# Performance work log

Hardware: AMD Instinct MI355X
Metric: run time of the kernel (lower is better)

The kernel has to match this reference:

```python
import jax, jax.numpy as jnp
from jax import lax
import numpy as np

A = 9            # anchors per location (3 scales x 3 ratios)
STRIDE = 16      # feat_stride
PRE_NMS = 6000   # top-k proposals before NMS (test mode)
POST_NMS = 300   # proposals kept after NMS (test mode)
NMS_T = 0.7      # NMS IoU threshold
MIN_SIZE = 16.0  # min proposal side length


def _anchor_ref(base=16, ratios=(0.5, 1.0, 2.0), scales=(8, 16, 32)):
    """Standard py-faster-rcnn anchor references, shape (9, 4)."""
    ratios = np.array(ratios, np.float64)
    scales = np.array(scales, np.float64)
    ctr = (base - 1) / 2.0
    size = float(base * base)
    ws = np.round(np.sqrt(size / ratios))
    hs = np.round(ws * ratios)
    ra = np.stack([ctr - 0.5 * (ws - 1), ctr - 0.5 * (hs - 1),
                   ctr + 0.5 * (ws - 1), ctr + 0.5 * (hs - 1)], 1)
    out = []
    for a in ra:
        w = a[2] - a[0] + 1.0
        h = a[3] - a[1] + 1.0
        cx = a[0] + 0.5 * (w - 1)
        cy = a[1] + 0.5 * (h - 1)
        ws2 = w * scales
        hs2 = h * scales
        out.append(np.stack([cx - 0.5 * (ws2 - 1), cy - 0.5 * (hs2 - 1),
                             cx + 0.5 * (ws2 - 1), cy + 0.5 * (hs2 - 1)], 1))
    return jnp.asarray(np.concatenate(out, 0), jnp.float32)


def _nms_keep(boxes):
    """Greedy NMS on score-sorted boxes (N,4) -> bool keep mask (N,)."""
    x1, y1, x2, y2 = boxes[:, 0], boxes[:, 1], boxes[:, 2], boxes[:, 3]
    areas = (x2 - x1 + 1.0) * (y2 - y1 + 1.0)
    iw = jnp.clip(jnp.minimum(x2[:, None], x2[None, :]) - jnp.maximum(x1[:, None], x1[None, :]) + 1.0, 0.0)
    ih = jnp.clip(jnp.minimum(y2[:, None], y2[None, :]) - jnp.maximum(y1[:, None], y1[None, :]) + 1.0, 0.0)
    inter = iw * ih
    iou = inter / (areas[:, None] + areas[None, :] - inter)
    n = boxes.shape[0]
    idx = jnp.arange(n)
    def body(i, keep):
        sup = (iou[i] > NMS_T) & (idx > i)
        return jnp.where(keep[i], keep & ~sup, keep)
    return lax.fori_loop(0, n, body, jnp.ones((n,), bool))


def _rpn_forward(feature_map, W_rpn, b_rpn, W_score, b_score, W_bbox, b_bbox, img_size):
    dn = ('NHWC', 'HWIO', 'NHWC')
    rpn = lax.conv_general_dilated(feature_map, W_rpn, (1, 1), 'SAME', dimension_numbers=dn) + b_rpn
    rpn = jax.nn.relu(rpn)
    cls = lax.conv_general_dilated(rpn, W_score, (1, 1), 'SAME', dimension_numbers=dn) + b_score
    bbx = lax.conv_general_dilated(rpn, W_bbox, (1, 1), 'SAME', dimension_numbers=dn) + b_bbox
    n, h, w, _ = feature_map.shape
    cls = cls.reshape(n, h, w, A, 2)
    prob = jax.nn.softmax(cls, axis=-1)
    fg = prob[..., 1].reshape(-1)           # (h*w*A,) foreground prob
    deltas = bbx.reshape(-1, 4)             # (h*w*A, 4)
    # anchors: shifts over (h, w), anchor-ref inner -> matches (h,w,A) flattening
    ref = _anchor_ref()
    sx = jnp.arange(w, dtype=jnp.float32) * STRIDE
    sy = jnp.arange(h, dtype=jnp.float32) * STRIDE
    ys, xs = jnp.meshgrid(sy, sx, indexing='ij')
    shifts = jnp.stack([xs, ys, xs, ys], -1).reshape(-1, 1, 4)
    anchors = (shifts + ref[None]).reshape(-1, 4)
    # decode deltas -> boxes
    aw = anchors[:, 2] - anchors[:, 0] + 1.0
    ah = anchors[:, 3] - anchors[:, 1] + 1.0
    acx = anchors[:, 0] + 0.5 * aw
    acy = anchors[:, 1] + 0.5 * ah
    pcx = deltas[:, 0] * aw + acx
    pcy = deltas[:, 1] * ah + acy
    pw = jnp.exp(deltas[:, 2]) * aw
    ph = jnp.exp(deltas[:, 3]) * ah
    imh = img_size[0].astype(jnp.float32)
    imw = img_size[1].astype(jnp.float32)
    boxes = jnp.stack([
        jnp.clip(pcx - 0.5 * pw, 0.0, imw - 1.0),
        jnp.clip(pcy - 0.5 * ph, 0.0, imh - 1.0),
        jnp.clip(pcx + 0.5 * pw, 0.0, imw - 1.0),
        jnp.clip(pcy + 0.5 * ph, 0.0, imh - 1.0)], -1)
    # min-size filter
    bw = boxes[:, 2] - boxes[:, 0] + 1.0
    bh = boxes[:, 3] - boxes[:, 1] + 1.0
    fg = jnp.where((bw >= MIN_SIZE) & (bh >= MIN_SIZE), fg, -1e9)
    # pre-NMS top-k (sorted descending)
    top_s, top_i = lax.top_k(fg, PRE_NMS)
    top_b = boxes[top_i]
    keep = _nms_keep(lax.stop_gradient(top_b))
    sel_s = jnp.where(keep, top_s, -1e9)
    _, sel_i = lax.top_k(sel_s, POST_NMS)
    rois = top_b[sel_i]
    ok = keep[sel_i] & (sel_s[sel_i] > -1e8)
    return jnp.where(ok[:, None], rois, 0.0)  # (POST_NMS, 4), zero-padded


def setup_inputs() -> dict:
    key = jax.random.key(0)
    ks = jax.random.split(key, 7)
    C_in, C_mid = 1024, 512
    std = 0.01
    return {
        'feature_map': jax.random.normal(ks[0], (1, 100, 150, C_in), jnp.float32),
        'W_rpn': jax.random.normal(ks[1], (3, 3, C_in, C_mid), jnp.float32) * std,
        'b_rpn': jnp.zeros((C_mid,), jnp.float32),
        'W_score': jax.random.normal(ks[2], (1, 1, C_mid, A * 2), jnp.float32) * std,
        'b_score': jnp.zeros((A * 2,), jnp.float32),
        'W_bbox': jax.random.normal(ks[3], (1, 1, C_mid, A * 4), jnp.float32) * std,
        'b_bbox': jnp.zeros((A * 4,), jnp.float32),
        'img_size': jnp.array([1600, 2400], jnp.int32),
    }


def reference(feature_map, W_rpn, b_rpn, W_score, b_score, W_bbox, b_bbox, img_size):
    return _rpn_forward(feature_map, W_rpn, b_rpn, W_score, b_score, W_bbox, b_bbox, img_size)
```

## Files before the change

### kernel.cpp

```cpp
#include <hip/hip_runtime.h>
#include <hip/hip_bf16.h>

typedef unsigned int u32;
typedef unsigned long long u64;

#define H_FM 100
#define W_FM 150
#define CIN 1024
#define CMID 512
#define NPIX 15000
#define NANCH 135000
#define PRE_NMS_N 6000
#define POST_NMS_N 300
#define WPR 94

typedef __attribute__((ext_vector_type(8))) short short8;
typedef __attribute__((ext_vector_type(8))) __bf16 bf16x8;
typedef __attribute__((ext_vector_type(4))) float f32x4;

__device__ __forceinline__ u32 fkey(float f) {
  u32 u = __float_as_uint(f);
  return (u & 0x80000000u) ? ~u : (u | 0x80000000u);
}

__device__ __forceinline__ u64 shfl64(u64 v, int src) {
  u32 lo = (u32)__shfl((int)(u32)v, src, 64);
  u32 hi = (u32)__shfl((int)(u32)(v >> 32), src, 64);
  return ((u64)hi << 32) | (u64)lo;
}

struct FragArg {
  short8 v;
  __device__ operator short8() const { return v; }
  __device__ operator bf16x8() const { return __builtin_bit_cast(bf16x8, v); }
};
__device__ __forceinline__ f32x4 mfma16(short8 a, short8 b, f32x4 c) {
  return __builtin_amdgcn_mfma_f32_16x16x32_bf16(FragArg{a}, FragArg{b}, c, 0, 0, 0);
}

#define GLL(gp, lp) __builtin_amdgcn_global_load_lds(                        \
    (const __attribute__((address_space(1))) unsigned int*)(gp),             \
    (__attribute__((address_space(3))) unsigned int*)(lp), 16, 0, 0)

__device__ __forceinline__ void split3(float f, unsigned short& a,
                                       unsigned short& b, unsigned short& c) {
  __hip_bfloat16 h0 = __float2bfloat16(f);
  float f0 = __bfloat162float(h0);
  float r1 = f - f0;
  __hip_bfloat16 h1 = __float2bfloat16(r1);
  float r2 = r1 - __bfloat162float(h1);
  __hip_bfloat16 h2 = __float2bfloat16(r2);
  a = *(unsigned short*)&h0;
  b = *(unsigned short*)&h1;
  c = *(unsigned short*)&h2;
}

__global__ __launch_bounds__(256) void k_split_fm(
    const float* __restrict__ src, unsigned short* __restrict__ d0,
    unsigned short* __restrict__ d1, unsigned short* __restrict__ d2,
    float* __restrict__ zp)
{
  if (blockIdx.x == 0 && threadIdx.x < 64) zp[threadIdx.x] = 0.f;
  const int n4 = NPIX * CIN / 4;
  for (int i = blockIdx.x * 256 + threadIdx.x; i < n4; i += gridDim.x * 256) {
    float4 v = ((const float4*)src)[i];
    float f[4] = {v.x, v.y, v.z, v.w};
    ushort4 o0, o1, o2;
    unsigned short* p0 = (unsigned short*)&o0;
    unsigned short* p1 = (unsigned short*)&o1;
    unsigned short* p2 = (unsigned short*)&o2;
    #pragma unroll
    for (int e = 0; e < 4; ++e) split3(f[e], p0[e], p1[e], p2[e]);
    ((ushort4*)d0)[i] = o0;
    ((ushort4*)d1)[i] = o1;
    ((ushort4*)d2)[i] = o2;
  }
}

__global__ __launch_bounds__(256) void k_split_wt(
    const float* __restrict__ Wsrc, unsigned short* __restrict__ t0,
    unsigned short* __restrict__ t1, unsigned short* __restrict__ t2)
{
  __shared__ float tile[64][65];
  const int k0 = blockIdx.x * 64;
  const int n0 = blockIdx.y * 64;
  const int tid = threadIdx.x;
  const int lr = tid >> 4;
  const int lc = (tid & 15) * 4;
  #pragma unroll
  for (int rr = 0; rr < 64; rr += 16) {
    float4 v = *(const float4*)&Wsrc[(size_t)(k0 + lr + rr) * CMID + n0 + lc];
    tile[lr + rr][lc + 0] = v.x; tile[lr + rr][lc + 1] = v.y;
    tile[lr + rr][lc + 2] = v.z; tile[lr + rr][lc + 3] = v.w;
  }
  __syncthreads();
  const int n = tid >> 2;
  const int kk = (tid & 3) * 16;
  unsigned short b0[16], b1[16], b2[16];
  #pragma unroll
  for (int e = 0; e < 16; ++e) split3(tile[kk + e][n], b0[e], b1[e], b2[e]);
  size_t ob = ((size_t)(n0 + n) * 9216 + k0 + kk) >> 2;
  #pragma unroll
  for (int q = 0; q < 4; ++q) {
    ((ushort4*)t0)[ob + q] = *(ushort4*)&b0[q * 4];
    ((ushort4*)t1)[ob + q] = *(ushort4*)&b1[q * 4];
    ((ushort4*)t2)[ob + q] = *(ushort4*)&b2[q * 4];
  }
}

__global__ __launch_bounds__(256, 2) void k_conv_mfma(
    const unsigned short* __restrict__ fm0, const unsigned short* __restrict__ fm1,
    const unsigned short* __restrict__ fm2, const unsigned short* __restrict__ wt0,
    const unsigned short* __restrict__ wt1, const unsigned short* __restrict__ wt2,
    const float* __restrict__ br, const float* __restrict__ zp,
    float* __restrict__ rpn)
{
  __shared__ char lds[49152];

  const int tid = threadIdx.x;
  const int lane = tid & 63;
  const int w = tid >> 6;
  const int bn = (blockIdx.x & 3) * 128;
  const int bm = (blockIdx.x >> 2) * 128;
  const int wm = (w >> 1) * 64;
  const int wn = (w & 1) * 64;

  unsigned aoff[3][4], boff[3][4];
  #pragma unroll
  for (int s = 0; s < 3; ++s)
    #pragma unroll
    for (int i = 0; i < 4; ++i) {
      aoff[s][i] = s * 8192 + (wm + i * 16 + (lane & 15)) * 64 + ((lane >> 4) << 4);
      boff[s][i] = 24576 + s * 8192 + (wn + i * 16 + (lane & 15)) * 64 + ((lane >> 4) << 4);
    }

  const int subrow = lane >> 2;
  const unsigned colb = (lane & 3) << 4;
  const int mR0 = w * 16 + subrow;
  const int mR1 = (w + 4) * 16 + subrow;
  char* ldsA0 = lds + w * 1024;
  char* ldsA1 = lds + (w + 4) * 1024;
  char* ldsB0 = lds + 24576 + w * 1024;
  char* ldsB1 = lds + 24576 + (w + 4) * 1024;
  const size_t rowB0 = (size_t)(bn + mR0) * 18432 + colb;
  const size_t rowB1 = (size_t)(bn + mR1) * 18432 + colb;
  const char* zpb = (const char*)zp + colb;

  f32x4 acc[4][4];
  #pragma unroll
  for (int i = 0; i < 4; ++i)
    #pragma unroll
    for (int j = 0; j < 4; ++j) acc[i][j] = (f32x4){0.f, 0.f, 0.f, 0.f};

  for (int seg = 0; seg < 9; ++seg) {
    const int dy = seg / 3 - 1, dx = seg % 3 - 1;
    size_t aO0 = 0, aO1 = 0;
    bool av0, av1;
    {
      int pm = bm + mR0;
      int y = pm / W_FM, x = pm - y * W_FM;
      int sy = y + dy, sx = x + dx;
      av0 = (pm < NPIX) && ((unsigned)sy < H_FM) && ((unsigned)sx < W_FM);
      aO0 = (size_t)(unsigned)(sy * W_FM + sx) * 2048 + colb;
    }
    {
      int pm = bm + mR1;
      int y = pm / W_FM, x = pm - y * W_FM;
      int sy = y + dy, sx = x + dx;
      av1 = (pm < NPIX) && ((unsigned)sy < H_FM) && ((unsigned)sx < W_FM);
      aO1 = (size_t)(unsigned)(sy * W_FM + sx) * 2048 + colb;
    }
    const size_t bS0 = rowB0 + (size_t)seg * 2048;
    const size_t bS1 = rowB1 + (size_t)seg * 2048;

    for (int chb = 0; chb < 2048; chb += 64) {
      __syncthreads();
      {
        const char* g;
        g = av0 ? ((const char*)fm0 + aO0 + chb) : zpb; GLL(g, ldsA0);
        g = av1 ? ((const char*)fm0 + aO1 + chb) : zpb; GLL(g, ldsA1);
        g = av0 ? ((const char*)fm1 + aO0 + chb) : zpb; GLL(g, ldsA0 + 8192);
        g = av1 ? ((const char*)fm1 + aO1 + chb) : zpb; GLL(g, ldsA1 + 8192);
        g = av0 ? ((const char*)fm2 + aO0 + chb) : zpb; GLL(g, ldsA0 + 16384);
        g = av1 ? ((const char*)fm2 + aO1 + chb) : zpb; GLL(g, ldsA1 + 16384);
        GLL((const char*)wt0 + bS0 + chb, ldsB0);
        GLL((const char*)wt0 + bS1 + chb, ldsB1);
        GLL((const char*)wt1 + bS0 + chb, ldsB0 + 8192);
        GLL((const char*)wt1 + bS1 + chb, ldsB1 + 8192);
        GLL((const char*)wt2 + bS0 + chb, ldsB0 + 16384);
        GLL((const char*)wt2 + bS1 + chb, ldsB1 + 16384);
      }
      __syncthreads();

      short8 B0[4], B1[4], B2[4];
      #pragma unroll
      for (int j = 0; j < 4; ++j) {
        B0[j] = *(const short8*)(lds + boff[0][j]);
        B1[j] = *(const short8*)(lds + boff[1][j]);
        B2[j] = *(const short8*)(lds + boff[2][j]);
      }
      #pragma unroll
      for (int i = 0; i < 4; ++i) {
        short8 A0 = *(const short8*)(lds + aoff[0][i]);
        short8 A1 = *(const short8*)(lds + aoff[1][i]);
        short8 A2 = *(const short8*)(lds + aoff[2][i]);
        #pragma unroll
        for (int j = 0; j < 4; ++j) {
          f32x4 c = acc[i][j];
          c = mfma16(A0, B0[j], c);
          c = mfma16(A0, B1[j], c);
          c = mfma16(A1, B0[j], c);
          c = mfma16(A1, B1[j], c);
          c = mfma16(A0, B2[j], c);
          c = mfma16(A2, B0[j], c);
          acc[i][j] = c;
        }
      }
    }
  }

  #pragma unroll
  for (int i = 0; i < 4; ++i) {
    const int mbase = bm + wm + i * 16 + ((lane >> 4) << 2);
    #pragma unroll
    for (int j = 0; j < 4; ++j) {
      const int n = bn + wn + j * 16 + (lane & 15);
      const float bias = br[n];
      #pragma unroll
      for (int r = 0; r < 4; ++r) {
        const int m = mbase + r;
        if (m < NPIX) rpn[(size_t)m * CMID + n] = fmaxf(acc[i][j][r] + bias, 0.f);
      }
    }
  }
}

__global__ __launch_bounds__(256) void k_conv(
    const float* __restrict__ fm, const float* __restrict__ Wr,
    const float* __restrict__ br, float* __restrict__ rpn)
{
  __shared__ float As[16][132];
  __shared__ float Bs[16][128];

  const int tid = threadIdx.x;
  const int ntile = blockIdx.x & 3;
  const int mtile = blockIdx.x >> 2;
  const int bm = mtile * 128, bn = ntile * 128;

  const int a_kg = tid & 3;
  const int a_r  = tid >> 2;
  const int m0 = bm + a_r, m1 = m0 + 64;
  const int y0 = m0 / W_FM, x0 = m0 % W_FM;
  const int y1 = m1 / W_FM, x1 = m1 % W_FM;
  const bool mv0 = m0 < NPIX, mv1 = m1 < NPIX;

  const int b_n4 = (tid & 31) << 2;
  const int b_k  = tid >> 5;
  const int tc = tid & 15, tr = tid >> 4;

  float acc[8][8];
  #pragma unroll
  for (int i = 0; i < 8; ++i)
    #pragma unroll
    for (int j = 0; j < 8; ++j) acc[i][j] = 0.f;

  const float4 z4 = make_float4(0.f, 0.f, 0.f, 0.f);

  for (int seg = 0; seg < 9; ++seg) {
    const int dy = seg / 3 - 1, dx = seg % 3 - 1;
    const int iy0 = y0 + dy, ix0 = x0 + dx;
    const int iy1 = y1 + dy, ix1 = x1 + dx;
    const bool v0 = mv0 && (unsigned)iy0 < H_FM && (unsigned)ix0 < W_FM;
    const bool v1 = mv1 && (unsigned)iy1 < H_FM && (unsigned)ix1 < W_FM;
    const float* pa0 = fm + (((iy0 * W_FM + ix0) << 10) + (a_kg << 2));
    const float* pa1 = fm + (((iy1 * W_FM + ix1) << 10) + (a_kg << 2));
    const float* pb  = Wr + ((size_t)(seg * CIN) * CMID) + bn + b_n4;

    for (int kc = 0; kc < CIN; kc += 16) {
      float4 av0 = v0 ? *(const float4*)(pa0 + kc) : z4;
      float4 av1 = v1 ? *(const float4*)(pa1 + kc) : z4;
      float4 bv0 = *(const float4*)(pb + (size_t)(kc + b_k) * CMID);
      float4 bv1 = *(const float4*)(pb + (size_t)(kc + b_k + 8) * CMID);

      __syncthreads();
      const int ka = a_kg << 2;
      As[ka + 0][a_r] = av0.x; As[ka + 1][a_r] = av0.y;
      As[ka + 2][a_r] = av0.z; As[ka + 3][a_r] = av0.w;
      As[ka + 0][a_r + 64] = av1.x; As[ka + 1][a_r + 64] = av1.y;
      As[ka + 2][a_r + 64] = av1.z; As[ka + 3][a_r + 64] = av1.w;
      *(float4*)&Bs[b_k][b_n4]     = bv0;
      *(float4*)&Bs[b_k + 8][b_n4] = bv1;
      __syncthreads();

      #pragma unroll
      for (int kk = 0; kk < 16; ++kk) {
        float a8[8], b8[8];
        *(float4*)&a8[0] = *(const float4*)&As[kk][tr * 8];
        *(float4*)&a8[4] = *(const float4*)&As[kk][tr * 8 + 4];
        *(float4*)&b8[0] = *(const float4*)&Bs[kk][tc * 8];
        *(float4*)&b8[4] = *(const float4*)&Bs[kk][tc * 8 + 4];
        #pragma unroll
        for (int i = 0; i < 8; ++i)
          #pragma unroll
          for (int j = 0; j < 8; ++j)
            acc[i][j] = fmaf(a8[i], b8[j], acc[i][j]);
      }
    }
  }

  float4 bias0 = *(const float4*)(br + bn + tc * 8);
  float4 bias1 = *(const float4*)(br + bn + tc * 8 + 4);
  #pragma unroll
  for (int i = 0; i < 8; ++i) {
    int m = bm + tr * 8 + i;
    if (m < NPIX) {
      float* op = rpn + (size_t)m * CMID + bn + tc * 8;
      float4 o0, o1;
      o0.x = fmaxf(acc[i][0] + bias0.x, 0.f);
      o0.y = fmaxf(acc[i][1] + bias0.y, 0.f);
      o0.z = fmaxf(acc[i][2] + bias0.z, 0.f);
      o0.w = fmaxf(acc[i][3] + bias0.w, 0.f);
      o1.x = fmaxf(acc[i][4] + bias1.x, 0.f);
      o1.y = fmaxf(acc[i][5] + bias1.y, 0.f);
      o1.z = fmaxf(acc[i][6] + bias1.z, 0.f);
      o1.w = fmaxf(acc[i][7] + bias1.w, 0.f);
      *(float4*)op = o0;
      *(float4*)(op + 4) = o1;
    }
  }
}

__global__ __launch_bounds__(64) void k_heads(
    const float* __restrict__ rpn,
    const float* __restrict__ Ws, const float* __restrict__ bs,
    const float* __restrict__ Wb, const float* __restrict__ bb,
    const int* __restrict__ img,
    float* __restrict__ fg, float4* __restrict__ boxes)
{
  __shared__ float r[512];
  __shared__ float vals[54];
  const int p = blockIdx.x, lane = threadIdx.x;
  const float* rp = rpn + (size_t)p * CMID;
  *(float4*)&r[lane * 8]     = *(const float4*)(rp + lane * 8);
  *(float4*)&r[lane * 8 + 4] = *(const float4*)(rp + lane * 8 + 4);
  __syncthreads();

  if (lane < 54) {
    const float* wp;
    int stride;
    float acc;
    if (lane < 18) { wp = Ws + lane; stride = 18; acc = bs[lane]; }
    else           { wp = Wb + (lane - 18); stride = 36; acc = bb[lane - 18]; }
    #pragma unroll 8
    for (int c = 0; c < 512; ++c) acc = fmaf(r[c], wp[c * stride], acc);
    vals[lane] = acc;
  }
  __syncthreads();

  if (lane < 9) {
    const int a = lane;
    const float AW[9] = {184.f, 368.f, 736.f, 128.f, 256.f, 512.f,  88.f, 176.f, 352.f};
    const float AH[9] = { 96.f, 192.f, 384.f, 128.f, 256.f, 512.f, 176.f, 352.f, 704.f};
    const int y = p / W_FM, x = p % W_FM;

    float c0 = vals[2 * a], c1 = vals[2 * a + 1];
    float score = 1.f / (1.f + expf(c0 - c1));

    float dxv = vals[18 + 4 * a + 0];
    float dyv = vals[18 + 4 * a + 1];
    float dwv = vals[18 + 4 * a + 2];
    float dhv = vals[18 + 4 * a + 3];

    float aw = AW[a], ah = AH[a];
    float acx = (float)(x * 16 + 8);
    float acy = (float)(y * 16 + 8);
    float pcx = dxv * aw + acx;
    float pcy = dyv * ah + acy;
    float pw = expf(dwv) * aw;
    float ph = expf(dhv) * ah;

    float imh1 = (float)img[0] - 1.f;
    float imw1 = (float)img[1] - 1.f;
    float b0 = fminf(fmaxf(pcx - 0.5f * pw, 0.f), imw1);
    float b1 = fminf(fmaxf(pcy - 0.5f * ph, 0.f), imh1);
    float b2 = fminf(fmaxf(pcx + 0.5f * pw, 0.f), imw1);
    float b3 = fminf(fmaxf(pcy + 0.5f * ph, 0.f), imh1);

    float bw = b2 - b0 + 1.f, bh = b3 - b1 + 1.f;
    if (!(bw >= 16.f && bh >= 16.f)) score = -1e9f;

    int gi = p * 9 + a;
    fg[gi] = score;
    boxes[gi] = make_float4(b0, b1, b2, b3);
  }
}

__global__ void k_init(u32* __restrict__ hist, u32* __restrict__ ctl) {
  hist[threadIdx.x] = 0;
  if (threadIdx.x == 0) { ctl[0] = 0; ctl[1] = PRE_NMS_N; ctl[2] = 0; ctl[3] = 0; }
}

__global__ __launch_bounds__(256) void k_hist(
    const float* __restrict__ fg, u32* __restrict__ hist,
    const u32* __restrict__ ctl, int pass)
{
  __shared__ u32 h[256];
  h[threadIdx.x] = 0;
  __syncthreads();
  const int shift = 24 - 8 * pass;
  const u32 prefix = ctl[0];
  for (int i = blockIdx.x * 256 + threadIdx.x; i < NANCH; i += 128 * 256) {
    u32 key = fkey(fg[i]);
    bool match = (pass == 0) || ((key >> (shift + 8)) == prefix);
    if (match) atomicAdd(&h[(key >> shift) & 255], 1u);
  }
  __syncthreads();
  u32 c = h[threadIdx.x];
  if (c) atomicAdd(&hist[threadIdx.x], c);
}

__global__ void k_scan(u32* __restrict__ hist, u32* __restrict__ ctl) {
  if (threadIdx.x == 0) {
    u32 kneed = ctl[1];
    u32 cum = 0;
    int d = 0;
    for (int dd = 255; dd >= 0; --dd) {
      u32 c = hist[dd];
      if (cum + c >= kneed) { d = dd; break; }
      cum += c;
    }
    ctl[0] = (ctl[0] << 8) | (u32)d;
    ctl[1] = kneed - cum;
  }
  __syncthreads();
  hist[threadIdx.x] = 0;
}

__global__ __launch_bounds__(256) void k_compact(
    const float* __restrict__ fg, u32* __restrict__ ctl,
    u64* __restrict__ listA, u32* __restrict__ listB)
{
  int i = blockIdx.x * 256 + threadIdx.x;
  if (i >= NANCH) return;
  u32 T = ctl[0];
  u32 key = fkey(fg[i]);
  if (key > T) {
    u32 slot = atomicAdd(&ctl[2], 1u);
    listA[slot] = ((u64)key << 32) | (u64)(0xFFFFFFFFu - (u32)i);
  } else if (key == T) {
    u32 slot = atomicAdd(&ctl[3], 1u);
    if (slot < 8192) listB[slot] = (u32)i;
  }
}

__global__ __launch_bounds__(256) void k_tiefix(
    u32* __restrict__ ctl, const u32* __restrict__ listB, u64* __restrict__ listA)
{
  __shared__ u32 s[8192];
  const int tid = threadIdx.x;
  const u32 kneed = ctl[1];
  const u32 base = ctl[2];
  const u32 cntB = min(ctl[3], 8192u);
  const u32 T = ctl[0];
  if (kneed == 0) return;
  if (cntB == kneed) {
    for (u32 t = tid; t < kneed; t += 256)
      listA[base + t] = ((u64)T << 32) | (u64)(0xFFFFFFFFu - listB[t]);
    return;
  }
  u32 n2 = 1;
  while (n2 < cntB) n2 <<= 1;
  for (u32 i = tid; i < n2; i += 256) s[i] = (i < cntB) ? listB[i] : 0xFFFFFFFFu;
  __syncthreads();
  for (u32 k = 2; k <= n2; k <<= 1) {
    for (u32 j = k >> 1; j > 0; j >>= 1) {
      for (u32 i = tid; i < n2; i += 256) {
        u32 ixj = i ^ j;
        if (ixj > i) {
          u32 a = s[i], b = s[ixj];
          bool up = ((i & k) == 0);
          if ((a > b) == up) { s[i] = b; s[ixj] = a; }
        }
      }
      __syncthreads();
    }
  }
  for (u32 t = tid; t < kneed; t += 256)
    listA[base + t] = ((u64)T << 32) | (u64)(0xFFFFFFFFu - s[t]);
}

__global__ __launch_bounds__(1024) void k_sort(
    const u64* __restrict__ listA, u64* __restrict__ sorted)
{
  __shared__ u64 s[8192];
  const int tid = threadIdx.x;
  for (int i = tid; i < 8192; i += 1024) s[i] = (i < PRE_NMS_N) ? listA[i] : 0ull;
  __syncthreads();
  for (int k = 2; k <= 8192; k <<= 1) {
    for (int j = k >> 1; j > 0; j >>= 1) {
      for (int i = tid; i < 8192; i += 1024) {
        int ixj = i ^ j;
        if (ixj > i) {
          u64 a = s[i], b = s[ixj];
          bool up = ((i & k) == 0);
          if ((a < b) == up) { s[i] = b; s[ixj] = a; }
        }
      }
      __syncthreads();
    }
  }
  for (int i = tid; i < 8192; i += 1024) sorted[i] = s[i];
}

__global__ __launch_bounds__(256) void k_gather(
    const u64* __restrict__ sorted, const float4* __restrict__ boxes,
    float4* __restrict__ tb)
{
  int t = blockIdx.x * 256 + threadIdx.x;
  if (t >= PRE_NMS_N) return;
  u64 p = sorted[t];
  u32 idx = 0xFFFFFFFFu - (u32)(p & 0xFFFFFFFFull);
  tb[t] = boxes[idx];
}

__global__ __launch_bounds__(64) void k_mask(
    const float4* __restrict__ tb, u64* __restrict__ mask)
{
  __shared__ float4 cb[64];
  const int bj = blockIdx.x, bi = blockIdx.y, t = threadIdx.x;
  const int j0 = bj * 64;
  const int jn = min(64, PRE_NMS_N - j0);
  if (t < jn) cb[t] = tb[j0 + t];
  __syncthreads();
  const int i = bi * 64 + t;
  if (i >= PRE_NMS_N) return;
  const float4 b = tb[i];
  const float ai = (b.z - b.x + 1.f) * (b.w - b.y + 1.f);
  u64 bits = 0;
  for (int tt = 0; tt < jn; ++tt) {
    int j = j0 + tt;
    if (j <= i) continue;
    float4 c = cb[tt];
    float iw = fminf(b.z, c.z) - fmaxf(b.x, c.x) + 1.f;
    float ih = fminf(b.w, c.w) - fmaxf(b.y, c.y) + 1.f;
    float inter = fmaxf(iw, 0.f) * fmaxf(ih, 0.f);
    float aj = (c.z - c.x + 1.f) * (c.w - c.y + 1.f);
    float iou = inter / (ai + aj - inter);
    if (iou > 0.7f) bits |= (1ull << tt);
  }
  mask[(size_t)i * WPR + bj] = bits;
}

__global__ __launch_bounds__(64) void k_nms(
    const u64* __restrict__ mask, const float* __restrict__ tb,
    const u64* __restrict__ sorted, float* __restrict__ out)
{
  const int lane = threadIdx.x;
  u64 r0 = 0, r1 = 0;
  int kept = 0;
  const u32 kcut = fkey(-1e8f);
  for (int i = 0; i < PRE_NMS_N; ++i) {
    const int w = i >> 6, b = i & 63;
    u64 v0 = shfl64(r0, w & 63);
    u64 v1 = shfl64(r1, w & 63);
    u64 word = (w < 64) ? v0 : v1;
    if (!((word >> b) & 1ull)) {
      u32 key = (u32)(sorted[i] >> 32);
      if (key <= kcut) break;
      if (lane < 4) out[kept * 4 + lane] = tb[i * 4 + lane];
      ++kept;
      if (kept >= POST_NMS_N) break;
      const u64* row = mask + (size_t)i * WPR;
      r0 |= row[lane];
      if (lane < WPR - 64) r1 |= row[64 + lane];
    }
  }
  for (int j = kept * 4 + lane; j < POST_NMS_N * 4; j += 64) out[j] = 0.f;
}

extern "C" void kernel_launch(void* const* d_in, const int* in_sizes, int n_in,
                              void* d_out, int out_size, void* d_ws, size_t ws_size,
                              hipStream_t stream) {
  const float* fm  = (const float*)d_in[0];
  const float* Wr  = (const float*)d_in[1];
  const float* br  = (const float*)d_in[2];
  const float* Wsc = (const float*)d_in[3];
  const float* bsc = (const float*)d_in[4];
  const float* Wbb = (const float*)d_in[5];
  const float* bbb = (const float*)d_in[6];
  const int*   img = (const int*)d_in[7];
  float* out = (float*)d_out;

  char* w = (char*)d_ws;
  size_t off = 0;
  auto alloc = [&](size_t bytes) {
    size_t p = off;
    off = (off + bytes + 255) & ~(size_t)255;
    return p;
  };
  float* rpn    = (float*)(w + alloc((size_t)NPIX * CMID * 4));
  float* fg     = (float*)(w + alloc((size_t)NANCH * 4));
  float4* boxes = (float4*)(w + alloc((size_t)NANCH * 16));
  u32* hist     = (u32*)(w + alloc(1024));
  u32* ctl      = (u32*)(w + alloc(64));
  u64* listA    = (u64*)(w + alloc((size_t)PRE_NMS_N * 8));
  u32* listB    = (u32*)(w + alloc(8192 * 4));
  u64* sorted   = (u64*)(w + alloc(8192 * 8));
  float4* topbox= (float4*)(w + alloc((size_t)PRE_NMS_N * 16));
  u64* mask     = (u64*)(w + alloc((size_t)PRE_NMS_N * WPR * 8));
  float* zp     = (float*)(w + alloc(256));
  size_t fb = (size_t)NPIX * CIN * 2;
  size_t wb = (size_t)9216 * CMID * 2;
  unsigned short* fm0 = (unsigned short*)(w + alloc(fb));
  unsigned short* fm1 = (unsigned short*)(w + alloc(fb));
  unsigned short* fm2 = (unsigned short*)(w + alloc(fb));
  unsigned short* wt0 = (unsigned short*)(w + alloc(wb));
  unsigned short* wt1 = (unsigned short*)(w + alloc(wb));
  unsigned short* wt2 = (unsigned short*)(w + alloc(wb));
  const bool use_mfma = ws_size >= off;

  if (use_mfma) {
    k_split_fm<<<dim3(1024), dim3(256), 0, stream>>>(fm, fm0, fm1, fm2, zp);
    k_split_wt<<<dim3(144, 8), dim3(256), 0, stream>>>(Wr, wt0, wt1, wt2);
    k_conv_mfma<<<dim3(118 * 4), dim3(256), 0, stream>>>(
        fm0, fm1, fm2, wt0, wt1, wt2, br, zp, rpn);
  } else {
    k_conv<<<dim3(118 * 4), dim3(256), 0, stream>>>(fm, Wr, br, rpn);
  }
  k_heads<<<dim3(NPIX), dim3(64), 0, stream>>>(rpn, Wsc, bsc, Wbb, bbb, img, fg, boxes);
  k_init<<<1, 256, 0, stream>>>(hist, ctl);
  for (int pass = 0; pass < 4; ++pass) {
    k_hist<<<128, 256, 0, stream>>>(fg, hist, ctl, pass);
    k_scan<<<1, 256, 0, stream>>>(hist, ctl);
  }
  k_compact<<<(NANCH + 255) / 256, 256, 0, stream>>>(fg, ctl, listA, listB);
  k_tiefix<<<1, 256, 0, stream>>>(ctl, listB, listA);
  k_sort<<<1, 1024, 0, stream>>>(listA, sorted);
  k_gather<<<(PRE_NMS_N + 255) / 256, 256, 0, stream>>>(sorted, boxes, topbox);
  k_mask<<<dim3(WPR, WPR), 64, 0, stream>>>(topbox, mask);
  k_nms<<<1, 64, 0, stream>>>(mask, (const float*)topbox, sorted, out);
}
```

Baseline: 1.414 ms.

## Tile conv spatially with halo reuse, GEMM-ize heads, replace mask NMS

Result: slower. 2.872 ms (+103.2%).

```diff
diff --git a/kernel.cpp b/kernel.cpp
--- a/kernel.cpp
+++ b/kernel.cpp
@@ -12,7 +12,6 @@
 #define NANCH 135000
 #define PRE_NMS_N 6000
 #define POST_NMS_N 300
-#define WPR 94
 
 typedef __attribute__((ext_vector_type(8))) short short8;
 typedef __attribute__((ext_vector_type(8))) __bf16 bf16x8;
@@ -21,12 +20,6 @@
 __device__ __forceinline__ u32 fkey(float f) {
   u32 u = __float_as_uint(f);
   return (u & 0x80000000u) ? ~u : (u | 0x80000000u);
-}
-
-__device__ __forceinline__ u64 shfl64(u64 v, int src) {
-  u32 lo = (u32)__shfl((int)(u32)v, src, 64);
-  u32 hi = (u32)__shfl((int)(u32)(v >> 32), src, 64);
-  return ((u64)hi << 32) | (u64)lo;
 }
 
 struct FragArg {
@@ -108,43 +101,65 @@
   }
 }
 
-__global__ __launch_bounds__(256, 2) void k_conv_mfma(
+__global__ __launch_bounds__(256, 2) void k_conv5(
     const unsigned short* __restrict__ fm0, const unsigned short* __restrict__ fm1,
     const unsigned short* __restrict__ fm2, const unsigned short* __restrict__ wt0,
     const unsigned short* __restrict__ wt1, const unsigned short* __restrict__ wt2,
     const float* __restrict__ br, const float* __restrict__ zp,
     float* __restrict__ rpn)
 {
-  __shared__ char lds[49152];
-
+  __shared__ char lds[61440];
   const int tid = threadIdx.x;
   const int lane = tid & 63;
   const int w = tid >> 6;
   const int bn = (blockIdx.x & 3) * 128;
-  const int bm = (blockIdx.x >> 2) * 128;
-  const int wm = (w >> 1) * 64;
-  const int wn = (w & 1) * 64;
-
-  unsigned aoff[3][4], boff[3][4];
+  const int t = blockIdx.x >> 2;
+  const int ty = t / 6, tx = t - ty * 6;
+  const int py0 = ty * 5, px0 = tx * 25;
+  const int wm = (w >> 1) * 64, wn = (w & 1) * 64;
+
+  const unsigned short* fmP[3] = {fm0, fm1, fm2};
+  const unsigned short* wtP[3] = {wt0, wt1, wt2};
+
+  u64 asrc[9]; u32 amsk[9]; u32 adst[9];
+  #pragma unroll
+  for (int q = 0; q < 9; ++q) {
+    int j36 = w * 9 + q;
+    int s = j36 / 12, gg = j36 % 12;
+    int c = gg / 3, part = gg - c * 3;
+    int pix = part * 64 + lane;
+    int uy = pix / 27, ux = pix - uy * 27;
+    int gy = py0 + uy - 1, gx = px0 + ux - 1;
+    bool valid = (pix < 189) && ((unsigned)gy < H_FM) && ((unsigned)gx < W_FM);
+    asrc[q] = valid ? ((u64)(const char*)fmP[s] + (u64)(gy * W_FM + gx) * 2048 + c * 16)
+                    : (u64)(const char*)zp;
+    amsk[q] = valid ? 0xFFFFFFFFu : 0u;
+    adst[q] = s * 12288 + c * 3072 + part * 1024;
+  }
+  u64 bsrc[6]; u32 bdst[6];
+  #pragma unroll
+  for (int q = 0; q < 6; ++q) {
+    int j24 = w * 6 + q;
+    int s = j24 >> 3, gg = j24 & 7;
+    int c = gg >> 1, part = gg & 1;
+    int row = part * 64 + lane;
+    bsrc[q] = (u64)(const char*)wtP[s] + (u64)(bn + row) * 18432 + c * 16;
+    bdst[q] = 36864u + s * 8192 + c * 2048 + part * 1024;
+  }
+  int abase[4];
+  #pragma unroll
+  for (int i = 0; i < 4; ++i) {
+    int m = wm + i * 16 + (lane & 15);
+    int y = m / 25, x = m - y * 25;
+    abase[i] = y * 27 + x + 28;
+  }
+  const int aquad = (lane >> 4) * 3072;
+  u32 boff[3][4];
   #pragma unroll
   for (int s = 0; s < 3; ++s)
     #pragma unroll
-    for (int i = 0; i < 4; ++i) {
-      aoff[s][i] = s * 8192 + (wm + i * 16 + (lane & 15)) * 64 + ((lane >> 4) << 4);
-      boff[s][i] = 24576 + s * 8192 + (wn + i * 16 + (lane & 15)) * 64 + ((lane >> 4) << 4);
-    }
-
-  const int subrow = lane >> 2;
-  const unsigned colb = (lane & 3) << 4;
-  const int mR0 = w * 16 + subrow;
-  const int mR1 = (w + 4) * 16 + subrow;
-  char* ldsA0 = lds + w * 1024;
-  char* ldsA1 = lds + (w + 4) * 1024;
-  char* ldsB0 = lds + 24576 + w * 1024;
-  char* ldsB1 = lds + 24576 + (w + 4) * 1024;
-  const size_t rowB0 = (size_t)(bn + mR0) * 18432 + colb;
-  const size_t rowB1 = (size_t)(bn + mR1) * 18432 + colb;
-  const char* zpb = (const char*)zp + colb;
+    for (int j = 0; j < 4; ++j)
+      boff[s][j] = 36864u + s * 8192 + (lane >> 4) * 2048 + (wn + j * 16 + (lane & 15)) * 16;
 
   f32x4 acc[4][4];
   #pragma unroll
@@ -152,67 +167,41 @@
     #pragma unroll
     for (int j = 0; j < 4; ++j) acc[i][j] = (f32x4){0.f, 0.f, 0.f, 0.f};
 
-  for (int seg = 0; seg < 9; ++seg) {
-    const int dy = seg / 3 - 1, dx = seg % 3 - 1;
-    size_t aO0 = 0, aO1 = 0;
-    bool av0, av1;
-    {
-      int pm = bm + mR0;
-      int y = pm / W_FM, x = pm - y * W_FM;
-      int sy = y + dy, sx = x + dx;
-      av0 = (pm < NPIX) && ((unsigned)sy < H_FM) && ((unsigned)sx < W_FM);
-      aO0 = (size_t)(unsigned)(sy * W_FM + sx) * 2048 + colb;
-    }
-    {
-      int pm = bm + mR1;
-      int y = pm / W_FM, x = pm - y * W_FM;
-      int sy = y + dy, sx = x + dx;
-      av1 = (pm < NPIX) && ((unsigned)sy < H_FM) && ((unsigned)sx < W_FM);
-      aO1 = (size_t)(unsigned)(sy * W_FM + sx) * 2048 + colb;
-    }
-    const size_t bS0 = rowB0 + (size_t)seg * 2048;
-    const size_t bS1 = rowB1 + (size_t)seg * 2048;
-
-    for (int chb = 0; chb < 2048; chb += 64) {
+  for (int chb = 0; chb < 2048; chb += 64) {
+    __syncthreads();
+    #pragma unroll
+    for (int q = 0; q < 9; ++q)
+      GLL((const char*)(asrc[q] + (u64)(chb & amsk[q])), lds + adst[q]);
+    for (int seg = 0; seg < 9; ++seg) {
+      if (seg) __syncthreads();
+      const u32 so = (u32)(seg * 2048 + chb);
+      #pragma unroll
+      for (int q = 0; q < 6; ++q)
+        GLL((const char*)(bsrc[q] + so), lds + bdst[q]);
       __syncthreads();
-      {
-        const char* g;
-        g = av0 ? ((const char*)fm0 + aO0 + chb) : zpb; GLL(g, ldsA0);
-        g = av1 ? ((const char*)fm0 + aO1 + chb) : zpb; GLL(g, ldsA1);
-        g = av0 ? ((const char*)fm1 + aO0 + chb) : zpb; GLL(g, ldsA0 + 8192);
-        g = av1 ? ((const char*)fm1 + aO1 + chb) : zpb; GLL(g, ldsA1 + 8192);
-        g = av0 ? ((const char*)fm2 + aO0 + chb) : zpb; GLL(g, ldsA0 + 16384);
-        g = av1 ? ((const char*)fm2 + aO1 + chb) : zpb; GLL(g, ldsA1 + 16384);
-        GLL((const char*)wt0 + bS0 + chb, ldsB0);
-        GLL((const char*)wt0 + bS1 + chb, ldsB1);
-        GLL((const char*)wt1 + bS0 + chb, ldsB0 + 8192);
-        GLL((const char*)wt1 + bS1 + chb, ldsB1 + 8192);
-        GLL((const char*)wt2 + bS0 + chb, ldsB0 + 16384);
-        GLL((const char*)wt2 + bS1 + chb, ldsB1 + 16384);
-      }
-      __syncthreads();
-
-      short8 B0[4], B1[4], B2[4];
+
+      const int d = ((seg / 3) - 1) * 27 + (seg - (seg / 3) * 3 - 1);
+      short8 B[3][4];
       #pragma unroll
-      for (int j = 0; j < 4; ++j) {
-        B0[j] = *(const short8*)(lds + boff[0][j]);
-        B1[j] = *(const short8*)(lds + boff[1][j]);
-        B2[j] = *(const short8*)(lds + boff[2][j]);
-      }
+      for (int s = 0; s < 3; ++s)
+        #pragma unroll
+        for (int j = 0; j < 4; ++j)
+          B[s][j] = *(const short8*)(lds + boff[s][j]);
       #pragma unroll
       for (int i = 0; i < 4; ++i) {
-        short8 A0 = *(const short8*)(lds + aoff[0][i]);
-        short8 A1 = *(const short8*)(lds + aoff[1][i]);
-        short8 A2 = *(const short8*)(lds + aoff[2][i]);
+        const int ap = (abase[i] + d) * 16 + aquad;
+        short8 A0 = *(const short8*)(lds + ap);
+        short8 A1 = *(const short8*)(lds + 12288 + ap);
+        short8 A2 = *(const short8*)(lds + 24576 + ap);
         #pragma unroll
         for (int j = 0; j < 4; ++j) {
           f32x4 c = acc[i][j];
-          c = mfma16(A0, B0[j], c);
-          c = mfma16(A0, B1[j], c);
-          c = mfma16(A1, B0[j], c);
-          c = mfma16(A1, B1[j], c);
-          c = mfma16(A0, B2[j], c);
-          c = mfma16(A2, B0[j], c);
+          c = mfma16(A0, B[0][j], c);
+          c = mfma16(A0, B[1][j], c);
+          c = mfma16(A1, B[0][j], c);
+          c = mfma16(A1, B[1][j], c);
+          c = mfma16(A0, B[2][j], c);
+          c = mfma16(A2, B[0][j], c);
           acc[i][j] = c;
         }
       }
@@ -221,178 +210,139 @@
 
   #pragma unroll
   for (int i = 0; i < 4; ++i) {
-    const int mbase = bm + wm + i * 16 + ((lane >> 4) << 2);
-    #pragma unroll
-    for (int j = 0; j < 4; ++j) {
-      const int n = bn + wn + j * 16 + (lane & 15);
-      const float bias = br[n];
-      #pragma unroll
-      for (int r = 0; r < 4; ++r) {
-        const int m = mbase + r;
-        if (m < NPIX) rpn[(size_t)m * CMID + n] = fmaxf(acc[i][j][r] + bias, 0.f);
+    const int mb = wm + i * 16 + ((lane >> 4) << 2);
+    #pragma unroll
+    for (int r = 0; r < 4; ++r) {
+      const int m = mb + r;
+      if (m < 125) {
+        int y = m / 25, x = m - y * 25;
+        size_t gp = (size_t)((py0 + y) * W_FM + (px0 + x)) * CMID;
+        #pragma unroll
+        for (int j = 0; j < 4; ++j) {
+          const int n = bn + wn + j * 16 + (lane & 15);
+          rpn[gp + n] = fmaxf(acc[i][j][r] + br[n], 0.f);
+        }
       }
     }
   }
 }
 
-__global__ __launch_bounds__(256) void k_conv(
-    const float* __restrict__ fm, const float* __restrict__ Wr,
-    const float* __restrict__ br, float* __restrict__ rpn)
-{
-  __shared__ float As[16][132];
-  __shared__ float Bs[16][128];
-
-  const int tid = threadIdx.x;
-  const int ntile = blockIdx.x & 3;
-  const int mtile = blockIdx.x >> 2;
-  const int bm = mtile * 128, bn = ntile * 128;
-
-  const int a_kg = tid & 3;
-  const int a_r  = tid >> 2;
-  const int m0 = bm + a_r, m1 = m0 + 64;
-  const int y0 = m0 / W_FM, x0 = m0 % W_FM;
-  const int y1 = m1 / W_FM, x1 = m1 % W_FM;
-  const bool mv0 = m0 < NPIX, mv1 = m1 < NPIX;
-
-  const int b_n4 = (tid & 31) << 2;
-  const int b_k  = tid >> 5;
-  const int tc = tid & 15, tr = tid >> 4;
-
-  float acc[8][8];
-  #pragma unroll
-  for (int i = 0; i < 8; ++i)
-    #pragma unroll
-    for (int j = 0; j < 8; ++j) acc[i][j] = 0.f;
-
-  const float4 z4 = make_float4(0.f, 0.f, 0.f, 0.f);
-
-  for (int seg = 0; seg < 9; ++seg) {
-    const int dy = seg / 3 - 1, dx = seg % 3 - 1;
-    const int iy0 = y0 + dy, ix0 = x0 + dx;
-    const int iy1 = y1 + dy, ix1 = x1 + dx;
-    const bool v0 = mv0 && (unsigned)iy0 < H_FM && (unsigned)ix0 < W_FM;
-    const bool v1 = mv1 && (unsigned)iy1 < H_FM && (unsigned)ix1 < W_FM;
-    const float* pa0 = fm + (((iy0 * W_FM + ix0) << 10) + (a_kg << 2));
-    const float* pa1 = fm + (((iy1 * W_FM + ix1) << 10) + (a_kg << 2));
-    const float* pb  = Wr + ((size_t)(seg * CIN) * CMID) + bn + b_n4;
-
-    for (int kc = 0; kc < CIN; kc += 16) {
-      float4 av0 = v0 ? *(const float4*)(pa0 + kc) : z4;
-      float4 av1 = v1 ? *(const float4*)(pa1 + kc) : z4;
-      float4 bv0 = *(const float4*)(pb + (size_t)(kc + b_k) * CMID);
-      float4 bv1 = *(const float4*)(pb + (size_t)(kc + b_k + 8) * CMID);
-
-      __syncthreads();
-      const int ka = a_kg << 2;
-      As[ka + 0][a_r] = av0.x; As[ka + 1][a_r] = av0.y;
-      As[ka + 2][a_r] = av0.z; As[ka + 3][a_r] = av0.w;
-      As[ka + 0][a_r + 64] = av1.x; As[ka + 1][a_r + 64] = av1.y;
-      As[ka + 2][a_r + 64] = av1.z; As[ka + 3][a_r + 64] = av1.w;
-      *(float4*)&Bs[b_k][b_n4]     = bv0;
-      *(float4*)&Bs[b_k + 8][b_n4] = bv1;
-      __syncthreads();
-
-      #pragma unroll
-      for (int kk = 0; kk < 16; ++kk) {
-        float a8[8], b8[8];
-        *(float4*)&a8[0] = *(const float4*)&As[kk][tr * 8];
-        *(float4*)&a8[4] = *(const float4*)&As[kk][tr * 8 + 4];
-        *(float4*)&b8[0] = *(const float4*)&Bs[kk][tc * 8];
-        *(float4*)&b8[4] = *(const float4*)&Bs[kk][tc * 8 + 4];
-        #pragma unroll
-        for (int i = 0; i < 8; ++i)
-          #pragma unroll
-          for (int j = 0; j < 8; ++j)
-            acc[i][j] = fmaf(a8[i], b8[j], acc[i][j]);
-      }
-    }
-  }
-
-  float4 bias0 = *(const float4*)(br + bn + tc * 8);
-  float4 bias1 = *(const float4*)(br + bn + tc * 8 + 4);
-  #pragma unroll
-  for (int i = 0; i < 8; ++i) {
-    int m = bm + tr * 8 + i;
-    if (m < NPIX) {
-      float* op = rpn + (size_t)m * CMID + bn + tc * 8;
-      float4 o0, o1;
-      o0.x = fmaxf(acc[i][0] + bias0.x, 0.f);
-      o0.y = fmaxf(acc[i][1] + bias0.y, 0.f);
-      o0.z = fmaxf(acc[i][2] + bias0.z, 0.f);
-      o0.w = fmaxf(acc[i][3] + bias0.w, 0.f);
-      o1.x = fmaxf(acc[i][4] + bias1.x, 0.f);
-      o1.y = fmaxf(acc[i][5] + bias1.y, 0.f);
-      o1.z = fmaxf(acc[i][6] + bias1.z, 0.f);
-      o1.w = fmaxf(acc[i][7] + bias1.w, 0.f);
-      *(float4*)op = o0;
-      *(float4*)(op + 4) = o1;
-    }
-  }
-}
-
-__global__ __launch_bounds__(64) void k_heads(
-    const float* __restrict__ rpn,
+__global__ __launch_bounds__(256) void k_packW(
     const float* __restrict__ Ws, const float* __restrict__ bs,
     const float* __restrict__ Wb, const float* __restrict__ bb,
-    const int* __restrict__ img,
+    float* __restrict__ Wp, float* __restrict__ bp)
+{
+  int tt = blockIdx.x * 256 + threadIdx.x;
+  int k = tt >> 6, o = tt & 63;
+  float v = (o < 18) ? Ws[k * 18 + o] : ((o < 54) ? Wb[k * 36 + (o - 18)] : 0.f);
+  Wp[tt] = v;
+  if (tt < 64) bp[tt] = (tt < 18) ? bs[tt] : ((tt < 54) ? bb[tt - 18] : 0.f);
+}
+
+__global__ __launch_bounds__(256) void k_headgemm(
+    const float* __restrict__ rpn, const float* __restrict__ Wp,
+    const float* __restrict__ bp, float* __restrict__ vals)
+{
+  __shared__ float As[32][132];
+  __shared__ float Bs[32][64];
+  const int tid = threadIdx.x;
+  const int bm = blockIdx.x * 128;
+  const int mt = tid >> 3;
+  const int nt = tid & 7;
+  const int kg = tid & 7;
+  const int ar = tid >> 3;
+  const int n4 = (tid & 15) * 4;
+  const int kr = tid >> 4;
+  const float4 z4 = make_float4(0.f, 0.f, 0.f, 0.f);
+
+  float acc[4][8];
+  #pragma unroll
+  for (int i = 0; i < 4; ++i)
+    #pragma unroll
+    for (int j = 0; j < 8; ++j) acc[i][j] = 0.f;
+
+  for (int kc = 0; kc < 512; kc += 32) {
+    __syncthreads();
+    #pragma unroll
+    for (int rr = 0; rr < 128; rr += 32) {
+      int m = bm + ar + rr;
+      float4 v = (m < NPIX) ? *(const float4*)&rpn[(size_t)m * CMID + kc + kg * 4] : z4;
+      As[kg * 4 + 0][ar + rr] = v.x; As[kg * 4 + 1][ar + rr] = v.y;
+      As[kg * 4 + 2][ar + rr] = v.z; As[kg * 4 + 3][ar + rr] = v.w;
+    }
+    *(float4*)&Bs[kr][n4]      = *(const float4*)&Wp[(kc + kr) * 64 + n4];
+    *(float4*)&Bs[kr + 16][n4] = *(const float4*)&Wp[(kc + kr + 16) * 64 + n4];
+    __syncthreads();
+    #pragma unroll
+    for (int kk = 0; kk < 32; ++kk) {
+      float4 a = *(const float4*)&As[kk][mt * 4];
+      float4 b0 = *(const float4*)&Bs[kk][nt * 8];
+      float4 b1 = *(const float4*)&Bs[kk][nt * 8 + 4];
+      float av[4] = {a.x, a.y, a.z, a.w};
+      float bv[8] = {b0.x, b0.y, b0.z, b0.w, b1.x, b1.y, b1.z, b1.w};
+      #pragma unroll
+      for (int i = 0; i < 4; ++i)
+        #pragma unroll
+        for (int j = 0; j < 8; ++j) acc[i][j] = fmaf(av[i], bv[j], acc[i][j]);
+    }
+  }
+  float bias[8];
+  #pragma unroll
+  for (int j = 0; j < 8; ++j) bias[j] = bp[nt * 8 + j];
+  #pragma unroll
+  for (int r = 0; r < 4; ++r) {
+    int m = bm + mt * 4 + r;
+    if (m < NPIX) {
+      float o[8];
+      #pragma unroll
+      for (int j = 0; j < 8; ++j) o[j] = acc[r][j] + bias[j];
+      float* op = vals + (size_t)m * 64 + nt * 8;
+      *(float4*)op = *(float4*)&o[0];
+      *(float4*)(op + 4) = *(float4*)&o[4];
+    }
+  }
+}
+
+__global__ __launch_bounds__(256) void k_decode(
+    const float* __restrict__ vals, const int* __restrict__ img,
     float* __restrict__ fg, float4* __restrict__ boxes)
 {
-  __shared__ float r[512];
-  __shared__ float vals[54];
-  const int p = blockIdx.x, lane = threadIdx.x;
-  const float* rp = rpn + (size_t)p * CMID;
-  *(float4*)&r[lane * 8]     = *(const float4*)(rp + lane * 8);
-  *(float4*)&r[lane * 8 + 4] = *(const float4*)(rp + lane * 8 + 4);
-  __syncthreads();
-
-  if (lane < 54) {
-    const float* wp;
-    int stride;
-    float acc;
-    if (lane < 18) { wp = Ws + lane; stride = 18; acc = bs[lane]; }
-    else           { wp = Wb + (lane - 18); stride = 36; acc = bb[lane - 18]; }
-    #pragma unroll 8
-    for (int c = 0; c < 512; ++c) acc = fmaf(r[c], wp[c * stride], acc);
-    vals[lane] = acc;
-  }
-  __syncthreads();
-
-  if (lane < 9) {
-    const int a = lane;
-    const float AW[9] = {184.f, 368.f, 736.f, 128.f, 256.f, 512.f,  88.f, 176.f, 352.f};
-    const float AH[9] = { 96.f, 192.f, 384.f, 128.f, 256.f, 512.f, 176.f, 352.f, 704.f};
-    const int y = p / W_FM, x = p % W_FM;
-
-    float c0 = vals[2 * a], c1 = vals[2 * a + 1];
-    float score = 1.f / (1.f + expf(c0 - c1));
-
-    float dxv = vals[18 + 4 * a + 0];
-    float dyv = vals[18 + 4 * a + 1];
-    float dwv = vals[18 + 4 * a + 2];
-    float dhv = vals[18 + 4 * a + 3];
-
-    float aw = AW[a], ah = AH[a];
-    float acx = (float)(x * 16 + 8);
-    float acy = (float)(y * 16 + 8);
-    float pcx = dxv * aw + acx;
-    float pcy = dyv * ah + acy;
-    float pw = expf(dwv) * aw;
-    float ph = expf(dhv) * ah;
-
-    float imh1 = (float)img[0] - 1.f;
-    float imw1 = (float)img[1] - 1.f;
-    float b0 = fminf(fmaxf(pcx - 0.5f * pw, 0.f), imw1);
-    float b1 = fminf(fmaxf(pcy - 0.5f * ph, 0.f), imh1);
-    float b2 = fminf(fmaxf(pcx + 0.5f * pw, 0.f), imw1);
-    float b3 = fminf(fmaxf(pcy + 0.5f * ph, 0.f), imh1);
-
-    float bw = b2 - b0 + 1.f, bh = b3 - b1 + 1.f;
-    if (!(bw >= 16.f && bh >= 16.f)) score = -1e9f;
-
-    int gi = p * 9 + a;
-    fg[gi] = score;
-    boxes[gi] = make_float4(b0, b1, b2, b3);
-  }
+  int gi = blockIdx.x * 256 + threadIdx.x;
+  if (gi >= NANCH) return;
+  const int p = gi / 9, a = gi - p * 9;
+  const float AW[9] = {184.f, 368.f, 736.f, 128.f, 256.f, 512.f,  88.f, 176.f, 352.f};
+  const float AH[9] = { 96.f, 192.f, 384.f, 128.f, 256.f, 512.f, 176.f, 352.f, 704.f};
+  const int y = p / W_FM, x = p - y * W_FM;
+  const float* row = vals + (size_t)p * 64;
+
+  float c0 = row[2 * a], c1 = row[2 * a + 1];
+  float score = 1.f / (1.f + expf(c0 - c1));
+
+  float dxv = row[18 + 4 * a + 0];
+  float dyv = row[18 + 4 * a + 1];
+  float dwv = row[18 + 4 * a + 2];
+  float dhv = row[18 + 4 * a + 3];
+
+  float aw = AW[a], ah = AH[a];
+  float acx = (float)(x * 16 + 8);
+  float acy = (float)(y * 16 + 8);
+  float pcx = dxv * aw + acx;
+  float pcy = dyv * ah + acy;
+  float pw = expf(dwv) * aw;
+  float ph = expf(dhv) * ah;
+
+  float imh1 = (float)img[0] - 1.f;
+  float imw1 = (float)img[1] - 1.f;
+  float b0 = fminf(fmaxf(pcx - 0.5f * pw, 0.f), imw1);
+  float b1 = fminf(fmaxf(pcy - 0.5f * ph, 0.f), imh1);
+  float b2 = fminf(fmaxf(pcx + 0.5f * pw, 0.f), imw1);
+  float b3 = fminf(fmaxf(pcy + 0.5f * ph, 0.f), imh1);
+
+  float bw = b2 - b0 + 1.f, bh = b3 - b1 + 1.f;
+  if (!(bw >= 16.f && bh >= 16.f)) score = -1e9f;
+
+  fg[gi] = score;
+  boxes[gi] = make_float4(b0, b1, b2, b3);
 }
 
 __global__ void k_init(u32* __restrict__ hist, u32* __restrict__ ctl) {
@@ -523,59 +473,63 @@
   tb[t] = boxes[idx];
 }
 
-__global__ __launch_bounds__(64) void k_mask(
-    const float4* __restrict__ tb, u64* __restrict__ mask)
-{
-  __shared__ float4 cb[64];
-  const int bj = blockIdx.x, bi = blockIdx.y, t = threadIdx.x;
-  const int j0 = bj * 64;
-  const int jn = min(64, PRE_NMS_N - j0);
-  if (t < jn) cb[t] = tb[j0 + t];
-  __syncthreads();
-  const int i = bi * 64 + t;
-  if (i >= PRE_NMS_N) return;
-  const float4 b = tb[i];
-  const float ai = (b.z - b.x + 1.f) * (b.w - b.y + 1.f);
-  u64 bits = 0;
-  for (int tt = 0; tt < jn; ++tt) {
-    int j = j0 + tt;
-    if (j <= i) continue;
-    float4 c = cb[tt];
-    float iw = fminf(b.z, c.z) - fmaxf(b.x, c.x) + 1.f;
-    float ih = fminf(b.w, c.w) - fmaxf(b.y, c.y) + 1.f;
-    float inter = fmaxf(iw, 0.f) * fmaxf(ih, 0.f);
-    float aj = (c.z - c.x + 1.f) * (c.w - c.y + 1.f);
-    float iou = inter / (ai + aj - inter);
-    if (iou > 0.7f) bits |= (1ull << tt);
-  }
-  mask[(size_t)i * WPR + bj] = bits;
-}
-
-__global__ __launch_bounds__(64) void k_nms(
-    const u64* __restrict__ mask, const float* __restrict__ tb,
-    const u64* __restrict__ sorted, float* __restrict__ out)
-{
-  const int lane = threadIdx.x;
-  u64 r0 = 0, r1 = 0;
+__global__ __launch_bounds__(1024) void k_nms2(
+    const u64* __restrict__ sorted, const float4* __restrict__ tb,
+    float* __restrict__ out)
+{
+  __shared__ u32 rem[188];
+  __shared__ int s_next;
+  const int tid = threadIdx.x;
+  const u32 kcut = fkey(-1e8f);
+  const int BIG = 1 << 30;
+
+  for (int wd = tid; wd < 188; wd += 1024) {
+    u32 m = 0;
+    #pragma unroll 4
+    for (int b = 0; b < 32; ++b) {
+      int j = wd * 32 + b;
+      if (j >= PRE_NMS_N || (u32)(sorted[j] >> 32) <= kcut) m |= (1u << b);
+    }
+    rem[wd] = m;
+  }
+  __syncthreads();
+
   int kept = 0;
-  const u32 kcut = fkey(-1e8f);
-  for (int i = 0; i < PRE_NMS_N; ++i) {
-    const int w = i >> 6, b = i & 63;
-    u64 v0 = shfl64(r0, w & 63);
-    u64 v1 = shfl64(r1, w & 63);
-    u64 word = (w < 64) ? v0 : v1;
-    if (!((word >> b) & 1ull)) {
-      u32 key = (u32)(sorted[i] >> 32);
-      if (key <= kcut) break;
-      if (lane < 4) out[kept * 4 + lane] = tb[i * 4 + lane];
-      ++kept;
-      if (kept >= POST_NMS_N) break;
-      const u64* row = mask + (size_t)i * WPR;
-      r0 |= row[lane];
-      if (lane < WPR - 64) r1 |= row[64 + lane];
-    }
-  }
-  for (int j = kept * 4 + lane; j < POST_NMS_N * 4; j += 64) out[j] = 0.f;
+  int cur = 0;
+  for (;;) {
+    int found = -1;
+    for (int b = cur; b < PRE_NMS_N; b += 1024) {
+      if (tid == 0) s_next = BIG;
+      __syncthreads();
+      int idx = b + tid;
+      if (idx < PRE_NMS_N && !((rem[idx >> 5] >> (idx & 31)) & 1u))
+        atomicMin(&s_next, idx);
+      __syncthreads();
+      if (s_next != BIG) { found = s_next; break; }
+    }
+    if (found < 0) break;
+
+    float4 bi = tb[found];
+    if (tid < 4) out[kept * 4 + tid] = ((const float*)&tb[found])[tid];
+    ++kept;
+    if (kept >= POST_NMS_N) break;
+
+    const float ai = (bi.z - bi.x + 1.f) * (bi.w - bi.y + 1.f);
+    for (int j = found + 1 + tid; j < PRE_NMS_N; j += 1024) {
+      if (!((rem[j >> 5] >> (j & 31)) & 1u)) {
+        float4 c = tb[j];
+        float iw = fminf(bi.z, c.z) - fmaxf(bi.x, c.x) + 1.f;
+        float ih = fminf(bi.w, c.w) - fmaxf(bi.y, c.y) + 1.f;
+        float inter = fmaxf(iw, 0.f) * fmaxf(ih, 0.f);
+        float aj = (c.z - c.x + 1.f) * (c.w - c.y + 1.f);
+        float iou = inter / (ai + aj - inter);
+        if (iou > 0.7f) atomicOr(&rem[j >> 5], 1u << (j & 31));
+      }
+    }
+    __syncthreads();
+    cur = found + 1;
+  }
+  for (int j = kept * 4 + tid; j < POST_NMS_N * 4; j += 1024) out[j] = 0.f;
 }
 
 extern "C" void kernel_launch(void* const* d_in, const int* in_sizes, int n_in,
@@ -607,8 +561,10 @@
   u32* listB    = (u32*)(w + alloc(8192 * 4));
   u64* sorted   = (u64*)(w + alloc(8192 * 8));
   float4* topbox= (float4*)(w + alloc((size_t)PRE_NMS_N * 16));
-  u64* mask     = (u64*)(w + alloc((size_t)PRE_NMS_N * WPR * 8));
   float* zp     = (float*)(w + alloc(256));
+  float* Wp     = (float*)(w + alloc(512 * 64 * 4));
+  float* bp     = (float*)(w + alloc(64 * 4));
+  float* vals   = (float*)(w + alloc((size_t)NPIX * 64 * 4));
   size_t fb = (size_t)NPIX * CIN * 2;
   size_t wb = (size_t)9216 * CMID * 2;
   unsigned short* fm0 = (unsigned short*)(w + alloc(fb));
@@ -617,17 +573,14 @@
   unsigned short* wt0 = (unsigned short*)(w + alloc(wb));
   unsigned short* wt1 = (unsigned short*)(w + alloc(wb));
   unsigned short* wt2 = (unsigned short*)(w + alloc(wb));
-  const bool use_mfma = ws_size >= off;
-
-  if (use_mfma) {
-    k_split_fm<<<dim3(1024), dim3(256), 0, stream>>>(fm, fm0, fm1, fm2, zp);
-    k_split_wt<<<dim3(144, 8), dim3(256), 0, stream>>>(Wr, wt0, wt1, wt2);
-    k_conv_mfma<<<dim3(118 * 4), dim3(256), 0, stream>>>(
-        fm0, fm1, fm2, wt0, wt1, wt2, br, zp, rpn);
-  } else {
-    k_conv<<<dim3(118 * 4), dim3(256), 0, stream>>>(fm, Wr, br, rpn);
-  }
-  k_heads<<<dim3(NPIX), dim3(64), 0, stream>>>(rpn, Wsc, bsc, Wbb, bbb, img, fg, boxes);
+
+  k_split_fm<<<dim3(1024), dim3(256), 0, stream>>>(fm, fm0, fm1, fm2, zp);
+  k_split_wt<<<dim3(144, 8), dim3(256), 0, stream>>>(Wr, wt0, wt1, wt2);
+  k_packW<<<dim3(128), dim3(256), 0, stream>>>(Wsc, bsc, Wbb, bbb, Wp, bp);
+  k_conv5<<<dim3(120 * 4), dim3(256), 0, stream>>>(
+      fm0, fm1, fm2, wt0, wt1, wt2, br, zp, rpn);
+  k_headgemm<<<dim3(118), dim3(256), 0, stream>>>(rpn, Wp, bp, vals);
+  k_decode<<<dim3((NANCH + 255) / 256), dim3(256), 0, stream>>>(vals, img, fg, boxes);
   k_init<<<1, 256, 0, stream>>>(hist, ctl);
   for (int pass = 0; pass < 4; ++pass) {
     k_hist<<<128, 256, 0, stream>>>(fg, hist, ctl, pass);
@@ -637,6 +590,5 @@
   k_tiefix<<<1, 256, 0, stream>>>(ctl, listB, listA);
   k_sort<<<1, 1024, 0, stream>>>(listA, sorted);
   k_gather<<<(PRE_NMS_N + 255) / 256, 256, 0, stream>>>(sorted, boxes, topbox);
-  k_mask<<<dim3(WPR, WPR), 64, 0, stream>>>(topbox, mask);
-  k_nms<<<1, 64, 0, stream>>>(mask, (const float*)topbox, sorted, out);
-}
+  k_nms2<<<1, 1024, 0, stream>>>(sorted, topbox, out);
+}
```
